# Optimization experiments

Hardware: AMD Instinct MI355X
Metric: run time of the kernel (lower is better)

## Reference

```python
import jax, jax.numpy as jnp
import numpy as np

B, T, C, H = 4, 2048, 768, 12
HS = C // H

def setup_inputs() -> dict:
    key = jax.random.key(0)
    ks = jax.random.split(key, 5)
    s = 0.02
    return {
        "x": jax.random.normal(ks[0], (B, T, C), jnp.float32),
        "W_attn": jax.random.normal(ks[1], (C, 3 * C), jnp.float32) * s,
        "b_attn": jnp.zeros((3 * C,), jnp.float32),
        "W_proj": jax.random.normal(ks[2], (C, C), jnp.float32) * s,
        "b_proj": jnp.zeros((C,), jnp.float32),
    }

def reference(x, W_attn, b_attn, W_proj, b_proj):
    Bz, Tz, Cz = x.shape
    qkv = x @ W_attn + b_attn                       # [B,T,3C]
    q, k, v = jnp.split(qkv, 3, axis=-1)
    # [B,T,C] -> [B,H,T,HS]
    def heads(t):
        return t.reshape(Bz, Tz, H, HS).transpose(0, 2, 1, 3)
    q, k, v = heads(q), heads(k), heads(v)
    scale = 1.0 / jnp.sqrt(jnp.asarray(HS, x.dtype))
    att = jnp.einsum("bhqd,bhkd->bhqk", q, k) * scale  # [B,H,T,T]
    causal = jnp.tril(jnp.ones((Tz, Tz), bool))
    att = jnp.where(causal[None, None], att, -jnp.inf)
    att = jax.nn.softmax(att, axis=-1)
    y = jnp.einsum("bhqk,bhkd->bhqd", att, v)       # [B,H,T,HS]
    y = y.transpose(0, 2, 1, 3).reshape(Bz, Tz, Cz)
    return y @ W_proj + b_proj
```

## Files before the change

### kernel.cpp

```cpp
#include <hip/hip_runtime.h>
#include <hip/hip_bf16.h>


typedef short s16x8 __attribute__((ext_vector_type(8)));
typedef float f32x4 __attribute__((ext_vector_type(4)));
typedef unsigned short u16x4 __attribute__((ext_vector_type(4)));
typedef unsigned short u16x8 __attribute__((ext_vector_type(8)));

#define MFMA16 __builtin_amdgcn_mfma_f32_16x16x32_bf16

__device__ __forceinline__ unsigned short f2bf(float f) {
    union { float f; unsigned u; } v; v.f = f;
    unsigned r = v.u + 0x7FFFu + ((v.u >> 16) & 1u);
    return (unsigned short)(r >> 16);
}

__device__ __forceinline__ void gload16(const unsigned short* g, unsigned short* l) {
    __builtin_amdgcn_global_load_lds(
        (__attribute__((address_space(1))) void*)(const void*)g,
        (__attribute__((address_space(3))) void*)l, 16, 0, 0);
}

__global__ __launch_bounds__(256) void cvt_f32_bf16(
    const float* __restrict__ src, unsigned short* __restrict__ dst, int n4)
{
    int i = blockIdx.x * 256 + threadIdx.x;
    if (i >= n4) return;
    float4 v = reinterpret_cast<const float4*>(src)[i];
    u16x4 o = { f2bf(v.x), f2bf(v.y), f2bf(v.z), f2bf(v.w) };
    reinterpret_cast<u16x4*>(dst)[i] = o;
}

__global__ __launch_bounds__(256) void cvt_transpose(
    const float* __restrict__ src, unsigned short* __restrict__ dst, int R, int C)
{
    __shared__ unsigned short tile[32][33];
    const int c0 = blockIdx.x * 32, r0 = blockIdx.y * 32;
    const int tx = threadIdx.x & 31, ty = threadIdx.x >> 5;
#pragma unroll
    for (int j = 0; j < 32; j += 8)
        tile[ty + j][tx] = f2bf(src[(size_t)(r0 + ty + j) * C + c0 + tx]);
    __syncthreads();
#pragma unroll
    for (int j = 0; j < 32; j += 8)
        dst[(size_t)(c0 + ty + j) * R + r0 + tx] = tile[tx][ty + j];
}

template<bool SCALEQ, bool OUT_BF16>
__global__ __launch_bounds__(256, 2) void gemm_bt(
    const unsigned short* __restrict__ A, const unsigned short* __restrict__ Bt,
    const float* __restrict__ bias, void* __restrict__ Cout,
    int M, int N, int K)
{
    __shared__ unsigned short lds_a[128 * 32];
    __shared__ unsigned short lds_b[128 * 32];

    const int tid = threadIdx.x, lane = tid & 63, w = tid >> 6;
    const int wr = w >> 1, wc = w & 1;
    const int m0 = blockIdx.y * 128, n0 = blockIdx.x * 128;
    const int lr = lane & 15, lg = lane >> 4;

    f32x4 acc[4][4];
#pragma unroll
    for (int mi = 0; mi < 4; ++mi)
#pragma unroll
        for (int ni = 0; ni < 4; ++ni)
            acc[mi][ni] = f32x4{0.f, 0.f, 0.f, 0.f};

    const int sr = tid >> 2, sc = (tid & 3) * 8;
    const unsigned short* Ap = A  + (size_t)(m0 + sr) * K + sc;
    const unsigned short* Aq = A  + (size_t)(m0 + 64 + sr) * K + sc;
    const unsigned short* Bp = Bt + (size_t)(n0 + sr) * K + sc;
    const unsigned short* Bq = Bt + (size_t)(n0 + 64 + sr) * K + sc;
    unsigned short* la0 = lds_a + (w << 9);
    unsigned short* la1 = lds_a + 2048 + (w << 9);
    unsigned short* lb0 = lds_b + (w << 9);
    unsigned short* lb1 = lds_b + 2048 + (w << 9);

    for (int k0 = 0; k0 < K; k0 += 32) {
        gload16(Ap + k0, la0);
        gload16(Aq + k0, la1);
        gload16(Bp + k0, lb0);
        gload16(Bq + k0, lb1);
        __syncthreads();

        s16x8 af[4], bfr[4];
#pragma unroll
        for (int mi = 0; mi < 4; ++mi)
            af[mi] = *reinterpret_cast<const s16x8*>(&lds_a[(wr * 64 + mi * 16 + lr) * 32 + lg * 8]);
#pragma unroll
        for (int ni = 0; ni < 4; ++ni)
            bfr[ni] = *reinterpret_cast<const s16x8*>(&lds_b[(wc * 64 + ni * 16 + lr) * 32 + lg * 8]);
#pragma unroll
        for (int mi = 0; mi < 4; ++mi)
#pragma unroll
            for (int ni = 0; ni < 4; ++ni)
                acc[mi][ni] = MFMA16(af[mi], bfr[ni], acc[mi][ni], 0, 0, 0);
        __syncthreads();
    }

#pragma unroll
    for (int ni = 0; ni < 4; ++ni) {
        int col = n0 + wc * 64 + ni * 16 + lr;
        float bs = bias[col];
        float scq = (SCALEQ && col < 768) ? 0.18033688011112042f : 1.0f;
#pragma unroll
        for (int mi = 0; mi < 4; ++mi)
#pragma unroll
            for (int r = 0; r < 4; ++r) {
                int row = m0 + wr * 64 + mi * 16 + lg * 4 + r;
                float v = (acc[mi][ni][r] + bs) * scq;
                if (OUT_BF16)
                    ((unsigned short*)Cout)[(size_t)row * N + col] = f2bf(v);
                else
                    ((float*)Cout)[(size_t)row * N + col] = v;
            }
    }
}

__global__ __launch_bounds__(256, 4) void attn_fwd(
    const unsigned short* __restrict__ qkv, unsigned short* __restrict__ att)
{
    __shared__ unsigned short lds_k[64 * 72];
    __shared__ unsigned short lds_v[64 * 72 + 64];
    __shared__ unsigned short lds_p[4][32 * 72];

    const int tid = threadIdx.x, lane = tid & 63, w = tid >> 6;
    const int lr = lane & 15, lg = lane >> 4;
    const int bh = blockIdx.x;
    const int qt = 15 - blockIdx.y;
    const int b = bh / 12, h = bh % 12;
    const size_t bT = (size_t)b * 2048;
    const int q0 = qt * 128;
    const int wq = q0 + w * 32;

    s16x8 qf[2][2];
#pragma unroll
    for (int mi = 0; mi < 2; ++mi) {
        const size_t qoff = (bT + wq + mi * 16 + lr) * 2304 + h * 64 + lg * 8;
        qf[mi][0] = *reinterpret_cast<const s16x8*>(qkv + qoff);
        qf[mi][1] = *reinterpret_cast<const s16x8*>(qkv + qoff + 32);
    }

    f32x4 o[2][4];
    f32x4 lsum[2];
#pragma unroll
    for (int mi = 0; mi < 2; ++mi) {
        lsum[mi] = f32x4{0.f, 0.f, 0.f, 0.f};
#pragma unroll
        for (int dt = 0; dt < 4; ++dt) o[mi][dt] = f32x4{0.f, 0.f, 0.f, 0.f};
    }

    const int sr = tid >> 2, sc = (tid & 3) * 16;
    const unsigned short* kbase = qkv + (bT + sr) * 2304 + 768 + h * 64 + sc;
    const unsigned short* vbase = qkv + (bT + sr) * 2304 + 1536 + h * 64 + sc;
    unsigned short* kdst = &lds_k[sr * 72 + sc];
    unsigned short* vdst = &lds_v[sc * 72 + ((sc >> 3) & 7) * 8 + sr];
    const int lrx = lr ^ ((lg & 1) << 3);
    const int nb16 = ((lg >> 1) & 1) << 4;
    const int rsel = ((lr >> 2) & 3) << 3;

    const int nkt = 2 * (qt + 1);

    u16x8 kr0, kr1, vr0, vr1;
    kr0 = *reinterpret_cast<const u16x8*>(kbase);
    kr1 = *reinterpret_cast<const u16x8*>(kbase + 8);
    vr0 = *reinterpret_cast<const u16x8*>(vbase);
    vr1 = *reinterpret_cast<const u16x8*>(vbase + 8);

    for (int kt = 0; kt < nkt; ++kt) {
        const int kv0 = kt * 64;
        *reinterpret_cast<u16x8*>(kdst)     = kr0;
        *reinterpret_cast<u16x8*>(kdst + 8) = kr1;
#pragma unroll
        for (int jj = 0; jj < 8; ++jj)
            vdst[jj * 72 + (jj >> 3) * 8] = vr0[jj];
#pragma unroll
        for (int jj = 8; jj < 16; ++jj)
            vdst[jj * 72 + (jj >> 3) * 8] = vr1[jj - 8];
        __syncthreads();

        {
            const int ktn = (kt + 1 < nkt) ? kt + 1 : kt;
            const size_t off = (size_t)(ktn * 64) * 2304;
            kr0 = *reinterpret_cast<const u16x8*>(kbase + off);
            kr1 = *reinterpret_cast<const u16x8*>(kbase + off + 8);
            vr0 = *reinterpret_cast<const u16x8*>(vbase + off);
            vr1 = *reinterpret_cast<const u16x8*>(vbase + off + 8);
        }

        if (kv0 <= wq + 31) {
            f32x4 sf[2][4];
#pragma unroll
            for (int mi = 0; mi < 2; ++mi)
#pragma unroll
                for (int n = 0; n < 4; ++n) sf[mi][n] = f32x4{0.f, 0.f, 0.f, 0.f};
#pragma unroll
            for (int kk = 0; kk < 2; ++kk)
#pragma unroll
                for (int n = 0; n < 4; ++n) {
                    s16x8 kf = *reinterpret_cast<const s16x8*>(&lds_k[(n * 16 + lr) * 72 + kk * 32 + lg * 8]);
                    sf[0][n] = MFMA16(qf[0][kk], kf, sf[0][n], 0, 0, 0);
                    sf[1][n] = MFMA16(qf[1][kk], kf, sf[1][n], 0, 0, 0);
                }

            if (kv0 + 63 > wq) {
#pragma unroll
                for (int mi = 0; mi < 2; ++mi)
#pragma unroll
                    for (int n = 0; n < 4; ++n)
#pragma unroll
                        for (int r = 0; r < 4; ++r) {
                            int key = kv0 + n * 16 + lr;
                            int row = wq + mi * 16 + lg * 4 + r;
                            if (key > row) sf[mi][n][r] = -1.0e30f;
                        }
            }

#pragma unroll
            for (int mi = 0; mi < 2; ++mi)
#pragma unroll
                for (int n = 0; n < 4; ++n) {
                    f32x4 p;
#pragma unroll
                    for (int r = 0; r < 4; ++r) p[r] = __builtin_amdgcn_exp2f(sf[mi][n][r]);
                    lsum[mi] += p;
                    const int kx = ((n << 4) ^ nb16) + lrx;
#pragma unroll
                    for (int r = 0; r < 4; ++r)
                        lds_p[w][(mi * 16 + lg * 4 + r) * 72 + kx] = f2bf(p[r]);
                }

#pragma unroll
            for (int kk = 0; kk < 2; ++kk) {
                const int pko = (kk * 32 + lg * 8) ^ rsel;
                s16x8 pf0 = *reinterpret_cast<const s16x8*>(&lds_p[w][lr * 72 + pko]);
                s16x8 pf1 = *reinterpret_cast<const s16x8*>(&lds_p[w][(16 + lr) * 72 + pko]);
#pragma unroll
                for (int dt = 0; dt < 4; ++dt) {
                    const int vrow = dt * 16 + lr;
                    s16x8 vf = *reinterpret_cast<const s16x8*>(
                        &lds_v[vrow * 72 + ((vrow >> 3) & 7) * 8 + kk * 32 + lg * 8]);
                    o[0][dt] = MFMA16(pf0, vf, o[0][dt], 0, 0, 0);
                    o[1][dt] = MFMA16(pf1, vf, o[1][dt], 0, 0, 0);
                }
            }
        }
        __syncthreads();
    }

#pragma unroll
    for (int mi = 0; mi < 2; ++mi)
#pragma unroll
        for (int mask = 1; mask < 16; mask <<= 1)
#pragma unroll
            for (int r = 0; r < 4; ++r)
                lsum[mi][r] += __shfl_xor(lsum[mi][r], mask);

#pragma unroll
    for (int mi = 0; mi < 2; ++mi)
#pragma unroll
        for (int dt = 0; dt < 4; ++dt)
#pragma unroll
            for (int r = 0; r < 4; ++r) {
                int row = wq + mi * 16 + lg * 4 + r;
                att[(bT + row) * 768 + h * 64 + dt * 16 + lr] = f2bf(o[mi][dt][r] / lsum[mi][r]);
            }
}

extern "C" void kernel_launch(void* const* d_in, const int* in_sizes, int n_in,
                              void* d_out, int out_size, void* d_ws, size_t ws_size,
                              hipStream_t stream) {
    const float* x      = (const float*)d_in[0];
    const float* W_attn = (const float*)d_in[1];
    const float* b_attn = (const float*)d_in[2];
    const float* W_proj = (const float*)d_in[3];
    const float* b_proj = (const float*)d_in[4];

    unsigned short* ws    = (unsigned short*)d_ws;
    unsigned short* x_bf  = ws;
    unsigned short* wa_t  = x_bf + 6291456;
    unsigned short* wp_t  = wa_t + 1769472;
    unsigned short* qkv   = wp_t + 589824;
    unsigned short* att   = qkv + 18874368;

    cvt_f32_bf16<<<6144, 256, 0, stream>>>(x, x_bf, 6291456 / 4);
    cvt_transpose<<<dim3(72, 24), 256, 0, stream>>>(W_attn, wa_t, 768, 2304);
    cvt_transpose<<<dim3(24, 24), 256, 0, stream>>>(W_proj, wp_t, 768, 768);

    gemm_bt<true , true ><<<dim3(18, 64), 256, 0, stream>>>(x_bf, wa_t, b_attn, qkv, 8192, 2304, 768);
    attn_fwd<<<dim3(48, 16), 256, 0, stream>>>(qkv, att);
    gemm_bt<false, false><<<dim3(6, 64), 256, 0, stream>>>(att, wp_t, b_proj, d_out, 8192, 768, 768);
}
```

Before: 223.2 us.

## Deepen GEMM K-tile with swizzled LDS, transpose QK^T MFMA, packed V/P stores

The GEMM now stages 64-wide K tiles into XOR-swizzled LDS and remaps block IDs so neighbouring blocks share tiles, which halves barrier count and is meant to cut bank conflicts and improve L2 reuse. The attention kernel swaps the MFMA operands for S so each lane holds four consecutive keys. That lets P be stored as packed 4-element vectors, and V is transposed into LDS with packed 32-bit writes and an XOR swizzle. MFMA sections get raised scheduling priority, the row-sum reduction uses fewer shuffles, and bf16 conversion uses the HIP intrinsic. Together these touch many parts of both kernels, adding LDS footprint in the GEMM and some index complexity.

Measured after the change: 225.3 us. No clear change (+1.0%).

```diff
diff --git a/kernel.cpp b/kernel.cpp
--- a/kernel.cpp
+++ b/kernel.cpp
@@ -10,9 +10,8 @@
 #define MFMA16 __builtin_amdgcn_mfma_f32_16x16x32_bf16
 
 __device__ __forceinline__ unsigned short f2bf(float f) {
-    union { float f; unsigned u; } v; v.f = f;
-    unsigned r = v.u + 0x7FFFu + ((v.u >> 16) & 1u);
-    return (unsigned short)(r >> 16);
+    __hip_bfloat16 h = __float2bfloat16(f);
+    return *reinterpret_cast<unsigned short*>(&h);
 }
 
 __device__ __forceinline__ void gload16(const unsigned short* g, unsigned short* l) {
@@ -52,13 +51,18 @@
     const float* __restrict__ bias, void* __restrict__ Cout,
     int M, int N, int K)
 {
-    __shared__ unsigned short lds_a[128 * 32];
-    __shared__ unsigned short lds_b[128 * 32];
+    __shared__ unsigned short lds_a[128 * 64];
+    __shared__ unsigned short lds_b[128 * 64];
 
     const int tid = threadIdx.x, lane = tid & 63, w = tid >> 6;
     const int wr = w >> 1, wc = w & 1;
-    const int m0 = blockIdx.y * 128, n0 = blockIdx.x * 128;
     const int lr = lane & 15, lg = lane >> 4;
+
+    const int nbx = gridDim.x;
+    const int bid = blockIdx.x + nbx * blockIdx.y;
+    const int cpx = (nbx * gridDim.y) >> 3;
+    const int swz = (bid & 7) * cpx + (bid >> 3);
+    const int m0 = (swz / nbx) * 128, n0 = (swz % nbx) * 128;
 
     f32x4 acc[4][4];
 #pragma unroll
@@ -67,35 +71,42 @@
         for (int ni = 0; ni < 4; ++ni)
             acc[mi][ni] = f32x4{0.f, 0.f, 0.f, 0.f};
 
-    const int sr = tid >> 2, sc = (tid & 3) * 8;
-    const unsigned short* Ap = A  + (size_t)(m0 + sr) * K + sc;
-    const unsigned short* Aq = A  + (size_t)(m0 + 64 + sr) * K + sc;
-    const unsigned short* Bp = Bt + (size_t)(n0 + sr) * K + sc;
-    const unsigned short* Bq = Bt + (size_t)(n0 + 64 + sr) * K + sc;
-    unsigned short* la0 = lds_a + (w << 9);
-    unsigned short* la1 = lds_a + 2048 + (w << 9);
-    unsigned short* lb0 = lds_b + (w << 9);
-    unsigned short* lb1 = lds_b + 2048 + (w << 9);
-
-    for (int k0 = 0; k0 < K; k0 += 32) {
-        gload16(Ap + k0, la0);
-        gload16(Aq + k0, la1);
-        gload16(Bp + k0, lb0);
-        gload16(Bq + k0, lb1);
+    const int srow = 8 * w + (lane >> 3);
+    const int sslot = ((lane & 7) ^ (lane >> 3)) * 8;
+    const unsigned short* Ap = A  + (size_t)(m0 + srow) * K + sslot;
+    const unsigned short* Bp = Bt + (size_t)(n0 + srow) * K + sslot;
+    unsigned short* la = lds_a + w * 512;
+    unsigned short* lb = lds_b + w * 512;
+
+    for (int k0 = 0; k0 < K; k0 += 64) {
+#pragma unroll
+        for (int p = 0; p < 4; ++p) {
+            gload16(Ap + (size_t)(32 * p) * K + k0, la + 2048 * p);
+            gload16(Bp + (size_t)(32 * p) * K + k0, lb + 2048 * p);
+        }
         __syncthreads();
 
-        s16x8 af[4], bfr[4];
-#pragma unroll
-        for (int mi = 0; mi < 4; ++mi)
-            af[mi] = *reinterpret_cast<const s16x8*>(&lds_a[(wr * 64 + mi * 16 + lr) * 32 + lg * 8]);
-#pragma unroll
-        for (int ni = 0; ni < 4; ++ni)
-            bfr[ni] = *reinterpret_cast<const s16x8*>(&lds_b[(wc * 64 + ni * 16 + lr) * 32 + lg * 8]);
-#pragma unroll
-        for (int mi = 0; mi < 4; ++mi)
-#pragma unroll
-            for (int ni = 0; ni < 4; ++ni)
-                acc[mi][ni] = MFMA16(af[mi], bfr[ni], acc[mi][ni], 0, 0, 0);
+#pragma unroll
+        for (int kh = 0; kh < 2; ++kh) {
+            s16x8 af[4], bfr[4];
+#pragma unroll
+            for (int mi = 0; mi < 4; ++mi) {
+                const int row = wr * 64 + mi * 16 + lr;
+                af[mi] = *reinterpret_cast<const s16x8*>(
+                    &lds_a[row * 64 + ((kh * 32 + lg * 8) ^ ((row & 7) << 3))]);
+            }
+#pragma unroll
+            for (int ni = 0; ni < 4; ++ni) {
+                const int row = wc * 64 + ni * 16 + lr;
+                bfr[ni] = *reinterpret_cast<const s16x8*>(
+                    &lds_b[row * 64 + ((kh * 32 + lg * 8) ^ ((row & 7) << 3))]);
+            }
+#pragma unroll
+            for (int mi = 0; mi < 4; ++mi)
+#pragma unroll
+                for (int ni = 0; ni < 4; ++ni)
+                    acc[mi][ni] = MFMA16(af[mi], bfr[ni], acc[mi][ni], 0, 0, 0);
+        }
         __syncthreads();
     }
 
@@ -122,7 +133,7 @@
     const unsigned short* __restrict__ qkv, unsigned short* __restrict__ att)
 {
     __shared__ unsigned short lds_k[64 * 72];
-    __shared__ unsigned short lds_v[64 * 72 + 64];
+    __shared__ unsigned short lds_v[64 * 72];
     __shared__ unsigned short lds_p[4][32 * 72];
 
     const int tid = threadIdx.x, lane = tid & 63, w = tid >> 6;
@@ -131,8 +142,7 @@
     const int qt = 15 - blockIdx.y;
     const int b = bh / 12, h = bh % 12;
     const size_t bT = (size_t)b * 2048;
-    const int q0 = qt * 128;
-    const int wq = q0 + w * 32;
+    const int wq = qt * 128 + w * 32;
 
     s16x8 qf[2][2];
 #pragma unroll
@@ -151,33 +161,30 @@
         for (int dt = 0; dt < 4; ++dt) o[mi][dt] = f32x4{0.f, 0.f, 0.f, 0.f};
     }
 
-    const int sr = tid >> 2, sc = (tid & 3) * 16;
-    const unsigned short* kbase = qkv + (bT + sr) * 2304 + 768 + h * 64 + sc;
-    const unsigned short* vbase = qkv + (bT + sr) * 2304 + 1536 + h * 64 + sc;
-    unsigned short* kdst = &lds_k[sr * 72 + sc];
-    unsigned short* vdst = &lds_v[sc * 72 + ((sc >> 3) & 7) * 8 + sr];
-    const int lrx = lr ^ ((lg & 1) << 3);
-    const int nb16 = ((lg >> 1) & 1) << 4;
-    const int rsel = ((lr >> 2) & 3) << 3;
+    const int ksr = tid >> 2, ksc = (tid & 3) * 16;
+    const unsigned short* kbase = qkv + (bT + ksr) * 2304 + 768 + h * 64 + ksc;
+    unsigned short* kdst = &lds_k[ksr * 72 + ksc];
+    const int vkp = tid >> 3, vdb = (tid & 7) * 8;
+    const unsigned short* vbase = qkv + (bT + 2 * vkp) * 2304 + 1536 + h * 64 + vdb;
 
     const int nkt = 2 * (qt + 1);
 
-    u16x8 kr0, kr1, vr0, vr1;
-    kr0 = *reinterpret_cast<const u16x8*>(kbase);
-    kr1 = *reinterpret_cast<const u16x8*>(kbase + 8);
-    vr0 = *reinterpret_cast<const u16x8*>(vbase);
-    vr1 = *reinterpret_cast<const u16x8*>(vbase + 8);
+    u16x8 kr0 = *reinterpret_cast<const u16x8*>(kbase);
+    u16x8 kr1 = *reinterpret_cast<const u16x8*>(kbase + 8);
+    u16x8 vr0 = *reinterpret_cast<const u16x8*>(vbase);
+    u16x8 vr1 = *reinterpret_cast<const u16x8*>(vbase + 2304);
 
     for (int kt = 0; kt < nkt; ++kt) {
         const int kv0 = kt * 64;
         *reinterpret_cast<u16x8*>(kdst)     = kr0;
         *reinterpret_cast<u16x8*>(kdst + 8) = kr1;
 #pragma unroll
-        for (int jj = 0; jj < 8; ++jj)
-            vdst[jj * 72 + (jj >> 3) * 8] = vr0[jj];
-#pragma unroll
-        for (int jj = 8; jj < 16; ++jj)
-            vdst[jj * 72 + (jj >> 3) * 8] = vr1[jj - 8];
+        for (int j = 0; j < 8; ++j) {
+            const int d = vdb + j;
+            unsigned pk = (unsigned)vr0[j] | ((unsigned)vr1[j] << 16);
+            *reinterpret_cast<unsigned*>(
+                &lds_v[d * 72 + ((2 * vkp) ^ (((d >> 3) & 7) << 3))]) = pk;
+        }
         __syncthreads();
 
         {
@@ -186,7 +193,7 @@
             kr0 = *reinterpret_cast<const u16x8*>(kbase + off);
             kr1 = *reinterpret_cast<const u16x8*>(kbase + off + 8);
             vr0 = *reinterpret_cast<const u16x8*>(vbase + off);
-            vr1 = *reinterpret_cast<const u16x8*>(vbase + off + 8);
+            vr1 = *reinterpret_cast<const u16x8*>(vbase + off + 2304);
         }
 
         if (kv0 <= wq + 31) {
@@ -195,14 +202,17 @@
             for (int mi = 0; mi < 2; ++mi)
 #pragma unroll
                 for (int n = 0; n < 4; ++n) sf[mi][n] = f32x4{0.f, 0.f, 0.f, 0.f};
+            __builtin_amdgcn_s_setprio(1);
 #pragma unroll
             for (int kk = 0; kk < 2; ++kk)
 #pragma unroll
                 for (int n = 0; n < 4; ++n) {
-                    s16x8 kf = *reinterpret_cast<const s16x8*>(&lds_k[(n * 16 + lr) * 72 + kk * 32 + lg * 8]);
-                    sf[0][n] = MFMA16(qf[0][kk], kf, sf[0][n], 0, 0, 0);
-                    sf[1][n] = MFMA16(qf[1][kk], kf, sf[1][n], 0, 0, 0);
+                    s16x8 kf = *reinterpret_cast<const s16x8*>(
+                        &lds_k[(n * 16 + lr) * 72 + kk * 32 + lg * 8]);
+                    sf[0][n] = MFMA16(kf, qf[0][kk], sf[0][n], 0, 0, 0);
+                    sf[1][n] = MFMA16(kf, qf[1][kk], sf[1][n], 0, 0, 0);
                 }
+            __builtin_amdgcn_s_setprio(0);
 
             if (kv0 + 63 > wq) {
 #pragma unroll
@@ -211,9 +221,9 @@
                     for (int n = 0; n < 4; ++n)
 #pragma unroll
                         for (int r = 0; r < 4; ++r) {
-                            int key = kv0 + n * 16 + lr;
-                            int row = wq + mi * 16 + lg * 4 + r;
-                            if (key > row) sf[mi][n][r] = -1.0e30f;
+                            int key = kv0 + n * 16 + 4 * lg + r;
+                            int qrow = wq + mi * 16 + lr;
+                            if (key > qrow) sf[mi][n][r] = -1.0e30f;
                         }
             }
 
@@ -225,46 +235,50 @@
 #pragma unroll
                     for (int r = 0; r < 4; ++r) p[r] = __builtin_amdgcn_exp2f(sf[mi][n][r]);
                     lsum[mi] += p;
-                    const int kx = ((n << 4) ^ nb16) + lrx;
-#pragma unroll
-                    for (int r = 0; r < 4; ++r)
-                        lds_p[w][(mi * 16 + lg * 4 + r) * 72 + kx] = f2bf(p[r]);
+                    u16x4 pk = { f2bf(p[0]), f2bf(p[1]), f2bf(p[2]), f2bf(p[3]) };
+                    *reinterpret_cast<u16x4*>(
+                        &lds_p[w][(mi * 16 + lr) * 72 + n * 16 + 4 * lg]) = pk;
                 }
 
+            __builtin_amdgcn_s_setprio(1);
 #pragma unroll
             for (int kk = 0; kk < 2; ++kk) {
-                const int pko = (kk * 32 + lg * 8) ^ rsel;
-                s16x8 pf0 = *reinterpret_cast<const s16x8*>(&lds_p[w][lr * 72 + pko]);
-                s16x8 pf1 = *reinterpret_cast<const s16x8*>(&lds_p[w][(16 + lr) * 72 + pko]);
+                s16x8 pf0 = *reinterpret_cast<const s16x8*>(
+                    &lds_p[w][lr * 72 + kk * 32 + lg * 8]);
+                s16x8 pf1 = *reinterpret_cast<const s16x8*>(
+                    &lds_p[w][(16 + lr) * 72 + kk * 32 + lg * 8]);
 #pragma unroll
                 for (int dt = 0; dt < 4; ++dt) {
                     const int vrow = dt * 16 + lr;
                     s16x8 vf = *reinterpret_cast<const s16x8*>(
-                        &lds_v[vrow * 72 + ((vrow >> 3) & 7) * 8 + kk * 32 + lg * 8]);
+                        &lds_v[vrow * 72 + ((kk * 32 + lg * 8) ^ (((vrow >> 3) & 7) << 3))]);
                     o[0][dt] = MFMA16(pf0, vf, o[0][dt], 0, 0, 0);
                     o[1][dt] = MFMA16(pf1, vf, o[1][dt], 0, 0, 0);
                 }
             }
+            __builtin_amdgcn_s_setprio(0);
         }
         __syncthreads();
     }
 
+    float inv[2];
+#pragma unroll
+    for (int mi = 0; mi < 2; ++mi) {
+        float s = lsum[mi][0] + lsum[mi][1] + lsum[mi][2] + lsum[mi][3];
+        s += __shfl_xor(s, 16);
+        s += __shfl_xor(s, 32);
+        inv[mi] = 1.0f / s;
+    }
+
 #pragma unroll
     for (int mi = 0; mi < 2; ++mi)
 #pragma unroll
-        for (int mask = 1; mask < 16; mask <<= 1)
-#pragma unroll
-            for (int r = 0; r < 4; ++r)
-                lsum[mi][r] += __shfl_xor(lsum[mi][r], mask);
-
-#pragma unroll
-    for (int mi = 0; mi < 2; ++mi)
-#pragma unroll
         for (int dt = 0; dt < 4; ++dt)
 #pragma unroll
             for (int r = 0; r < 4; ++r) {
-                int row = wq + mi * 16 + lg * 4 + r;
-                att[(bT + row) * 768 + h * 64 + dt * 16 + lr] = f2bf(o[mi][dt][r] / lsum[mi][r]);
+                int qrow = wq + mi * 16 + 4 * lg + r;
+                float sc = __shfl(inv[mi], 4 * lg + r);
+                att[(bT + qrow) * 768 + h * 64 + dt * 16 + lr] = f2bf(o[mi][dt][r] * sc);
             }
 }
 
```
